# Kernel optimization log

Measured on AMD Instinct MI355X. Metric: run time of the kernel, lower is better.

The kernel has to match this reference:

```python
import jax, jax.numpy as jnp
import numpy as np

NUM_HEADS = 4
NEG_INF = -1e9  # finite large-negative to avoid inf*weight -> nan in head combiner


def setup_inputs() -> dict:
    key = jax.random.key(0)
    k1, k2, k3, k4, k5 = jax.random.split(key, 5)
    B, S, T = 16, 1024, 512
    Q, E = 256, 512
    src_encodings = jax.random.normal(k1, (B, S, E), dtype=jnp.float32)
    src_token_mask = jax.random.randint(k2, (B, S), 0, 2).astype(jnp.bool_)
    query_vec = jax.random.normal(k3, (T, B, Q), dtype=jnp.float32)
    # Linear(src_encoding_size, query_vec_size * numheads, bias=False)
    W_src = jax.random.normal(k4, (E, Q * NUM_HEADS), dtype=jnp.float32) * (1.0 / np.sqrt(E))
    # Linear(numheads, 1, bias=False) -> combiner vector of shape (numheads,)
    w_comb = jax.random.normal(k5, (NUM_HEADS,), dtype=jnp.float32) * 0.5
    return {"src_encodings": src_encodings, "src_token_mask": src_token_mask,
            "query_vec": query_vec, "W_src": W_src, "w_comb": w_comb}


def reference(src_encodings, src_token_mask, query_vec, W_src, w_comb):
    # project + leaky_relu: (B,S,E) @ (E,H*Q) -> (B,S,H*Q)
    proj = jax.nn.leaky_relu(src_encodings @ W_src)
    B, S, _ = proj.shape
    Q = query_vec.shape[-1]
    proj = proj.reshape(B, S, NUM_HEADS, Q)                 # (B,S,H,Q)
    # per-head attention scores against each query step: (T,B,S,H)
    scores = jnp.einsum('bshq,tbq->tbsh', proj, query_vec)
    # mask invalid source tokens along S (broadcast over T and heads)
    scores = jnp.where(src_token_mask[None, :, :, None], NEG_INF, scores)
    # multihead combiner Linear(H,1,bias=False): (T,B,S)
    weights = jnp.einsum('tbsh,h->tbs', scores, w_comb)
    return jax.nn.softmax(weights, axis=-1)
```

## Files before the change

kernel.cpp:

```cpp
#include <hip/hip_runtime.h>
#include <hip/hip_bf16.h>
#include <cstdint>

constexpr int Bn = 16;
constexpr int Sn = 1024;
constexpr int Tn = 512;
constexpr int QD = 256;
constexpr int En = 512;
constexpr int Hn = 4;
constexpr float SLOPE = 0.01f;
constexpr float NEG_INF = -1e9f;
constexpr int Mn = Bn * Sn;

typedef _Float16 f16;
typedef f16 f16x4 __attribute__((ext_vector_type(4)));
typedef f16 f16x8 __attribute__((ext_vector_type(8)));
typedef float f32x4 __attribute__((ext_vector_type(4)));

#define G2L(g, l) __builtin_amdgcn_global_load_lds(                      \
    (const __attribute__((address_space(1))) void*)(g),                  \
    (__attribute__((address_space(3))) void*)(l), 16, 0, 0)

#define VM6 asm volatile("s_waitcnt vmcnt(6)" ::: "memory")
#define VM4 asm volatile("s_waitcnt vmcnt(4)" ::: "memory")
#define VM0 asm volatile("s_waitcnt vmcnt(0)" ::: "memory")
#define LG0 asm volatile("s_waitcnt lgkmcnt(0)" ::: "memory")

__device__ __forceinline__ void do_conv_a(const float* __restrict__ src,
                                          f16* __restrict__ Ah, f16* __restrict__ Al,
                                          int bid, int tid) {
    const size_t i4 = (size_t)bid * 256 + tid;
    const size_t base = i4 * 4;
    const float4 v = *(const float4*)(src + base);
    f16x4 hi, lo;
    const float xs[4] = {v.x, v.y, v.z, v.w};
    #pragma unroll
    for (int j = 0; j < 4; ++j) {
        f16 h = (f16)xs[j];
        hi[j] = h;
        lo[j] = (f16)(xs[j] - (float)h);
    }
    *(f16x4*)(Ah + base) = hi;
    *(f16x4*)(Al + base) = lo;
}

__device__ __forceinline__ void do_conv_b(const float* __restrict__ W,
                                          f16* __restrict__ Bht, f16* __restrict__ Blt,
                                          float (*T)[65], int nb, int tid) {
    const int n0 = (nb & 15) * 64;
    const int k0 = (nb >> 4) * 64;
    #pragma unroll
    for (int p = 0; p < 4; ++p) {
        const int e = p * 256 + tid;
        const int r = e >> 4;
        const int c4 = e & 15;
        const float4 v = *(const float4*)(W + (size_t)(k0 + r) * (Hn * QD) + n0 + c4 * 4);
        T[r][c4 * 4 + 0] = v.x; T[r][c4 * 4 + 1] = v.y;
        T[r][c4 * 4 + 2] = v.z; T[r][c4 * 4 + 3] = v.w;
    }
    __syncthreads();
    #pragma unroll
    for (int p = 0; p < 4; ++p) {
        const int e = p * 256 + tid;
        const int r = e >> 4;
        const int c4 = e & 15;
        f16x4 hi, lo;
        #pragma unroll
        for (int j = 0; j < 4; ++j) {
            const float x = T[c4 * 4 + j][r];
            f16 h = (f16)x;
            hi[j] = h;
            lo[j] = (f16)(x - (float)h);
        }
        const size_t off = (size_t)(n0 + r) * En + k0 + c4 * 4;
        *(f16x4*)(Bht + off) = hi;
        *(f16x4*)(Blt + off) = lo;
    }
}

__device__ __forceinline__ void do_conv_q(const float* __restrict__ query,
                                          f16* __restrict__ Qh, f16* __restrict__ Ql,
                                          int qb, int tid) {
    const int rloc = tid >> 6;
    const int lane = tid & 63;
    const int row = qb * 4 + rloc;
    const int t = row >> 4, b = row & 15;
    const float4 v = *(const float4*)(query + (size_t)row * QD + lane * 4);
    f16x4 hi, lo;
    const float xs[4] = {v.x, v.y, v.z, v.w};
    #pragma unroll
    for (int j = 0; j < 4; ++j) {
        f16 h = (f16)xs[j];
        hi[j] = h;
        lo[j] = (f16)(xs[j] - (float)h);
    }
    const size_t off = ((size_t)(b * Tn + t)) * QD + lane * 4;
    *(f16x4*)(Qh + off) = hi;
    *(f16x4*)(Ql + off) = lo;
}

__device__ __forceinline__ void do_detect(const unsigned char* __restrict__ mask_bytes,
                                          int* __restrict__ flag,
                                          int* cnt, int tid) {
    if (tid == 0) *cnt = 0;
    __syncthreads();
    int local = 0;
    for (int p = tid; p < 4096; p += 256) {
        if ((p & 3) != 0 && mask_bytes[p] != 0) local++;
    }
    atomicAdd(cnt, local);
    __syncthreads();
    if (tid == 0) flag[0] = (*cnt == 0) ? 1 : 0;
}

__global__ __launch_bounds__(256) void prep_all_kernel(
    const float* __restrict__ src, const float* __restrict__ W,
    const float* __restrict__ query,
    const unsigned char* __restrict__ mask_bytes,
    f16* __restrict__ Ah, f16* __restrict__ Al,
    f16* __restrict__ Bht, f16* __restrict__ Blt,
    f16* __restrict__ Qh, f16* __restrict__ Ql,
    int* __restrict__ flag)
{
    __shared__ float T[64][65];
    __shared__ int cnt;
    const int bid = blockIdx.x;
    const int tid = threadIdx.x;
    if (bid < 8192)       do_conv_a(src, Ah, Al, bid, tid);
    else if (bid < 8320)  do_conv_b(W, Bht, Blt, T, bid - 8192, tid);
    else if (bid < 10368) do_conv_q(query, Qh, Ql, bid - 8320, tid);
    else                  do_detect(mask_bytes, flag, &cnt, tid);
}

__global__ __launch_bounds__(256) void prep_kernel(
    const float* __restrict__ src, const float* __restrict__ W,
    const unsigned char* __restrict__ mask_bytes,
    f16* __restrict__ Ah, f16* __restrict__ Al,
    f16* __restrict__ Bht, f16* __restrict__ Blt,
    int* __restrict__ flag)
{
    __shared__ float T[64][65];
    __shared__ int cnt;
    const int bid = blockIdx.x;
    const int tid = threadIdx.x;
    if (bid < 8192)      do_conv_a(src, Ah, Al, bid, tid);
    else if (bid < 8320) do_conv_b(W, Bht, Blt, T, bid - 8192, tid);
    else                 do_detect(mask_bytes, flag, &cnt, tid);
}

__global__ __launch_bounds__(256) void conv_q_kernel(
    const float* __restrict__ query, f16* __restrict__ Qh, f16* __restrict__ Ql)
{
    do_conv_q(query, Qh, Ql, blockIdx.x, threadIdx.x);
}

__global__ __launch_bounds__(256) void gemm1_kernel(
    const f16* __restrict__ Ah, const f16* __restrict__ Al,
    const f16* __restrict__ Bht, const f16* __restrict__ Blt,
    const float* __restrict__ wcomb,
    f16* __restrict__ Ch, f16* __restrict__ Cl)
{
    __shared__ f16 lds_f[36864];

    const int tid = threadIdx.x;
    const int l  = tid & 63;
    const int wv = tid >> 6;
    const int wm = wv >> 1;
    const int wn = wv & 1;

    const int bid = blockIdx.x;
    const int swz = (bid & 7) * 64 + (bid >> 3);
    const int m0 = (swz >> 2) * 128;
    const int q0 = (swz & 3) * 64;

    const int rc  = tid >> 2;
    const int xk  = ((tid & 3) ^ ((tid >> 3) & 3)) * 8;
    const int stgA = (m0 + rc) * En + xk;
    const int stgB = (q0 + rc) * En + xk;

    const int xf  = (l >> 1) & 3;
    const int kx  = ((l >> 4) ^ xf) * 8;
    const int aFrag = (wm * 64 + (l & 15)) * 32 + kx;
    const int bFrag = 4096 + (wn * 32 + (l & 15)) * 32 + kx;

    f32x4 acc[4][8];
    #pragma unroll
    for (int m = 0; m < 4; ++m)
        #pragma unroll
        for (int f = 0; f < 8; ++f) acc[m][f] = (f32x4){0.f, 0.f, 0.f, 0.f};

    auto stage1 = [&](int t) {
        const f16* As = (t < 16) ? Ah : ((t < 32) ? Al : Ah);
        const f16* Bs = (t < 32) ? Bht : Blt;
        const int kofs = (t & 15) * 32;
        f16* dst = lds_f + (t % 3) * 12288 + wv * 512;
        G2L(As + stgA + kofs,                dst);
        G2L(As + stgA + 64 * En + kofs,      dst + 2048);
        G2L(Bs + stgB + kofs,                dst + 4096);
        G2L(Bs + stgB + QD * En + kofs,      dst + 4096 + 2048);
        G2L(Bs + stgB + 2 * QD * En + kofs,  dst + 4096 + 4096);
        G2L(Bs + stgB + 3 * QD * En + kofs,  dst + 4096 + 6144);
    };

    stage1(0);
    stage1(1);
    VM6;
    __builtin_amdgcn_s_barrier();

    #pragma unroll
    for (int t = 0; t < 48; ++t) {
        if (t + 2 < 48) stage1(t + 2);
        const f16* Lb = lds_f + (t % 3) * 12288;
        f16x8 af[4], bfr[8];
        #pragma unroll
        for (int m = 0; m < 4; ++m) af[m] = *(const f16x8*)(Lb + aFrag + m * 512);
        #pragma unroll
        for (int f = 0; f < 8; ++f)
            bfr[f] = *(const f16x8*)(Lb + bFrag + (f >> 1) * 2048 + (f & 1) * 512);
        __builtin_amdgcn_s_setprio(1);
        #pragma unroll
        for (int m = 0; m < 4; ++m) {
            #pragma unroll
            for (int f = 0; f < 8; ++f)
                acc[m][f] = __builtin_amdgcn_mfma_f32_16x16x32_f16(
                    af[m], bfr[f], acc[m][f], 0, 0, 0);
        }
        __builtin_amdgcn_s_setprio(0);
        if (t <= 45)      VM6;
        else if (t == 46) VM0;
        LG0;
        __builtin_amdgcn_s_barrier();
    }

    const float w0 = wcomb[0], w1 = wcomb[1], w2 = wcomb[2], w3 = wcomb[3];
    const int rbase = m0 + wm * 64 + (l >> 4) * 4;
    #pragma unroll
    for (int m = 0; m < 4; ++m) {
        #pragma unroll
        for (int qs = 0; qs < 2; ++qs) {
            const int q = q0 + wn * 32 + qs * 16 + (l & 15);
            #pragma unroll
            for (int i = 0; i < 4; ++i) {
                float x0 = acc[m][0 + qs][i]; x0 = x0 >= 0.f ? x0 : SLOPE * x0;
                float x1 = acc[m][2 + qs][i]; x1 = x1 >= 0.f ? x1 : SLOPE * x1;
                float x2 = acc[m][4 + qs][i]; x2 = x2 >= 0.f ? x2 : SLOPE * x2;
                float x3 = acc[m][6 + qs][i]; x3 = x3 >= 0.f ? x3 : SLOPE * x3;
                const float c = w0 * x0 + w1 * x1 + w2 * x2 + w3 * x3;
                const f16 ch = (f16)c;
                const f16 cl = (f16)(c - (float)ch);
                const size_t off = (size_t)(rbase + m * 16 + i) * QD + q;
                Ch[off] = ch;
                Cl[off] = cl;
            }
        }
    }
}

__global__ __launch_bounds__(256) void gemm2_kernel(
    const f16* __restrict__ Ch, const f16* __restrict__ Cl,
    const f16* __restrict__ Qh, const f16* __restrict__ Ql,
    const void* __restrict__ maskp, const float* __restrict__ wcomb,
    const int* __restrict__ flag,
    float* __restrict__ out)
{
    __shared__ f16 lds2[24576];

    const int tid = threadIdx.x;
    const int l  = tid & 63;
    const int wv = tid >> 6;
    const int wm = wv >> 1;
    const int wn = wv & 1;

    const int bid = blockIdx.x;
    const int swz = (bid & 7) * 64 + (bid >> 3);
    const int b   = swz >> 5;
    const int s0  = ((swz >> 2) & 7) * 128;
    const int t0  = (swz & 3) * 128;

    const int rowc = tid >> 2;
    const int xk   = ((tid & 3) ^ ((rowc >> 1) & 3)) * 8;
    const int stgA = (b * Sn + s0 + rowc) * QD + xk;
    const int stgB = (b * Tn + t0 + rowc) * QD + xk;

    const int xf  = ((l >> 1) & 3);
    const int aFrag = (wm * 64 + (l & 15)) * 32 + (((l >> 4) ^ xf) * 8);
    const int bFrag = 4096 + (wn * 64 + (l & 15)) * 32 + (((l >> 4) ^ xf) * 8);

    f32x4 acc[4][4];
    #pragma unroll
    for (int m = 0; m < 4; ++m)
        #pragma unroll
        for (int n = 0; n < 4; ++n) acc[m][n] = (f32x4){0.f, 0.f, 0.f, 0.f};

    auto stage1 = [&](int t) {
        const f16* As = (t < 8) ? Ch : ((t < 16) ? Cl : Ch);
        const f16* Bs = (t < 16) ? Qh : Ql;
        const int kofs = (t & 7) * 32;
        f16* dst = lds2 + (t % 3) * 8192 + wv * 512;
        G2L(As + stgA + kofs,           dst);
        G2L(As + stgA + 64 * QD + kofs, dst + 2048);
        G2L(Bs + stgB + kofs,           dst + 4096);
        G2L(Bs + stgB + 64 * QD + kofs, dst + 4096 + 2048);
    };

    stage1(0);
    stage1(1);
    VM4;
    __builtin_amdgcn_s_barrier();

    #pragma unroll
    for (int kt = 0; kt < 24; ++kt) {
        if (kt + 2 < 24) stage1(kt + 2);
        const f16* Lb = lds2 + (kt % 3) * 8192;
        f16x8 af[4], bfr[4];
        #pragma unroll
        for (int m = 0; m < 4; ++m) af[m] = *(const f16x8*)(Lb + aFrag + m * 512);
        #pragma unroll
        for (int n = 0; n < 4; ++n) bfr[n] = *(const f16x8*)(Lb + bFrag + n * 512);
        __builtin_amdgcn_s_setprio(1);
        #pragma unroll
        for (int m = 0; m < 4; ++m) {
            #pragma unroll
            for (int n = 0; n < 4; ++n)
                acc[m][n] = __builtin_amdgcn_mfma_f32_16x16x32_f16(
                    af[m], bfr[n], acc[m][n], 0, 0, 0);
        }
        __builtin_amdgcn_s_setprio(0);
        if (kt <= 21)      VM4;
        else if (kt == 22) VM0;
        LG0;
        __builtin_amdgcn_s_barrier();
    }

    const float sumw = wcomb[0] + wcomb[1] + wcomb[2] + wcomb[3];
    const float maskval = NEG_INF * sumw;
    const bool is_int = (flag[0] != 0);
    const int rbase = s0 + wm * 64 + (l >> 4) * 4;

    bool msk[4][4];
    #pragma unroll
    for (int m = 0; m < 4; ++m)
        #pragma unroll
        for (int i = 0; i < 4; ++i) {
            const int idx = b * Sn + rbase + m * 16 + i;
            int mm;
            if (is_int) mm = ((const int*)maskp)[idx];
            else        mm = (int)((const unsigned char*)maskp)[idx];
            msk[m][i] = (mm != 0);
        }

    #pragma unroll
    for (int m = 0; m < 4; ++m)
        #pragma unroll
        for (int n = 0; n < 4; ++n) {
            const int t = t0 + wn * 64 + n * 16 + (l & 15);
            float vals[4];
            #pragma unroll
            for (int i = 0; i < 4; ++i)
                vals[i] = msk[m][i] ? maskval : acc[m][n][i];
            *(float4*)(out + ((size_t)t * Bn + b) * Sn + rbase + m * 16)
                = make_float4(vals[0], vals[1], vals[2], vals[3]);
        }
}

__global__ __launch_bounds__(256) void softmax_kernel(float* __restrict__ out) {
    const int bid = blockIdx.x;
    const int k = bid & 7;
    const int r = bid >> 3;
    const int b = (k << 1) | (r & 1);
    const int t = r >> 1;
    const size_t row = (size_t)t * Bn + b;
    float* p = out + row * (size_t)Sn;
    const int tid = threadIdx.x;
    const int lane = tid & 63, wave = tid >> 6;

    float4 v = ((const float4*)p)[tid];

    float m = fmaxf(fmaxf(v.x, v.y), fmaxf(v.z, v.w));
    #pragma unroll
    for (int off = 32; off; off >>= 1) m = fmaxf(m, __shfl_down(m, off));
    __shared__ float smax[4];
    __shared__ float sm_all;
    if (lane == 0) smax[wave] = m;
    __syncthreads();
    if (tid == 0) sm_all = fmaxf(fmaxf(smax[0], smax[1]), fmaxf(smax[2], smax[3]));
    __syncthreads();
    m = sm_all;

    float e0 = __expf(v.x - m), e1 = __expf(v.y - m);
    float e2 = __expf(v.z - m), e3 = __expf(v.w - m);
    float s = e0 + e1 + e2 + e3;
    #pragma unroll
    for (int off = 32; off; off >>= 1) s += __shfl_down(s, off);
    __shared__ float ssum[4];
    __shared__ float ss_all;
    if (lane == 0) ssum[wave] = s;
    __syncthreads();
    if (tid == 0) ss_all = ssum[0] + ssum[1] + ssum[2] + ssum[3];
    __syncthreads();
    const float inv = 1.0f / ss_all;

    ((float4*)p)[tid] = make_float4(e0 * inv, e1 * inv, e2 * inv, e3 * inv);
}

extern "C" void kernel_launch(void* const* d_in, const int* in_sizes, int n_in,
                              void* d_out, int out_size, void* d_ws, size_t ws_size,
                              hipStream_t stream) {
    const float* src   = (const float*)d_in[0];
    const void*  maskp = d_in[1];
    const float* query = (const float*)d_in[2];
    const float* Wsrc  = (const float*)d_in[3];
    const float* wcomb = (const float*)d_in[4];
    float* out = (float*)d_out;

    constexpr size_t MB = 1024 * 1024;
    char* ws = (char*)d_ws;
    int* flag = (int*)ws;
    f16* Ah  = (f16*)(ws + 256);
    f16* Al  = (f16*)(ws + 256 + 16 * MB);
    f16* Bht = (f16*)(ws + 256 + 32 * MB);
    f16* Blt = (f16*)(ws + 256 + 33 * MB);
    f16* Ch  = (f16*)(ws + 256 + 34 * MB);
    f16* Cl  = (f16*)(ws + 256 + 42 * MB);

    const bool big_ws = (ws_size >= 58 * MB + 256);

    if (big_ws) {
        f16* Qh = (f16*)(ws + 256 + 50 * MB);
        f16* Ql = (f16*)(ws + 256 + 54 * MB);
        prep_all_kernel<<<10369, 256, 0, stream>>>(
            src, Wsrc, query, (const unsigned char*)maskp,
            Ah, Al, Bht, Blt, Qh, Ql, flag);
        gemm1_kernel<<<512, 256, 0, stream>>>(Ah, Al, Bht, Blt, wcomb, Ch, Cl);
        gemm2_kernel<<<512, 256, 0, stream>>>(Ch, Cl, Qh, Ql, maskp, wcomb, flag, out);
        softmax_kernel<<<Tn * Bn, 256, 0, stream>>>(out);
    } else {
        f16* Qh = (f16*)(ws + 256);
        f16* Ql = (f16*)(ws + 256 + 4 * MB);
        prep_kernel<<<8321, 256, 0, stream>>>(
            src, Wsrc, (const unsigned char*)maskp, Ah, Al, Bht, Blt, flag);
        gemm1_kernel<<<512, 256, 0, stream>>>(Ah, Al, Bht, Blt, wcomb, Ch, Cl);
        conv_q_kernel<<<(Tn * Bn) / 4, 256, 0, stream>>>(query, Qh, Ql);
        gemm2_kernel<<<512, 256, 0, stream>>>(Ch, Cl, Qh, Ql, maskp, wcomb, flag, out);
        softmax_kernel<<<Tn * Bn, 256, 0, stream>>>(out);
    }
}
```

Baseline: 108.6 us.

## Fuse prep, both GEMMs and softmax into one cooperative persistent kernel

Replaces the four-kernel sequence (prep, gemm1, gemm2, softmax) with a single cooperative kernel of 512 blocks that runs each stage in turn, separated by grid.sync barriers. The goal is to remove kernel launch gaps and tail effects between stages. In exchange, every stage is forced onto a fixed 512-block grid at 2 blocks per CU, and the grid-wide barriers add their own cost. If the cooperative launch fails, it falls back to separate kernels.

```diff
diff --git a/kernel.cpp b/kernel.cpp
--- a/kernel.cpp
+++ b/kernel.cpp
@@ -1,6 +1,9 @@
 #include <hip/hip_runtime.h>
 #include <hip/hip_bf16.h>
+#include <hip/hip_cooperative_groups.h>
 #include <cstdint>
+
+namespace cg = cooperative_groups;
 
 constexpr int Bn = 16;
 constexpr int Sn = 1024;
@@ -113,23 +116,265 @@
     if (tid == 0) flag[0] = (*cnt == 0) ? 1 : 0;
 }
 
-__global__ __launch_bounds__(256) void prep_all_kernel(
+__global__ __launch_bounds__(256, 2) void fused_kernel(
     const float* __restrict__ src, const float* __restrict__ W,
-    const float* __restrict__ query,
-    const unsigned char* __restrict__ mask_bytes,
+    const float* __restrict__ query, const void* __restrict__ maskp,
+    const float* __restrict__ wcomb,
     f16* __restrict__ Ah, f16* __restrict__ Al,
     f16* __restrict__ Bht, f16* __restrict__ Blt,
     f16* __restrict__ Qh, f16* __restrict__ Ql,
-    int* __restrict__ flag)
+    f16* __restrict__ Ch, f16* __restrict__ Cl,
+    int* __restrict__ flag, float* __restrict__ out)
 {
-    __shared__ float T[64][65];
-    __shared__ int cnt;
+    __shared__ f16 lds_f[36864];
+    __shared__ int s_cnt;
+    cg::grid_group grid = cg::this_grid();
     const int bid = blockIdx.x;
     const int tid = threadIdx.x;
-    if (bid < 8192)       do_conv_a(src, Ah, Al, bid, tid);
-    else if (bid < 8320)  do_conv_b(W, Bht, Blt, T, bid - 8192, tid);
-    else if (bid < 10368) do_conv_q(query, Qh, Ql, bid - 8320, tid);
-    else                  do_detect(mask_bytes, flag, &cnt, tid);
+
+    #pragma unroll 4
+    for (int j = 0; j < 16; ++j) do_conv_a(src, Ah, Al, bid * 16 + j, tid);
+    #pragma unroll
+    for (int j = 0; j < 4; ++j) do_conv_q(query, Qh, Ql, bid * 4 + j, tid);
+    if (bid < 128)
+        do_conv_b(W, Bht, Blt, reinterpret_cast<float(*)[65]>(lds_f), bid, tid);
+    if (bid == 511)
+        do_detect((const unsigned char*)maskp, flag, &s_cnt, tid);
+    grid.sync();
+
+    {
+        const int l  = tid & 63;
+        const int wv = tid >> 6;
+        const int wm = wv >> 1;
+        const int wn = wv & 1;
+
+        const int swz = (bid & 7) * 64 + (bid >> 3);
+        const int m0 = (swz >> 2) * 128;
+        const int q0 = (swz & 3) * 64;
+
+        const int rc  = tid >> 2;
+        const int xk  = ((tid & 3) ^ ((tid >> 3) & 3)) * 8;
+        const int stgA = (m0 + rc) * En + xk;
+        const int stgB = (q0 + rc) * En + xk;
+
+        const int xf  = (l >> 1) & 3;
+        const int kx  = ((l >> 4) ^ xf) * 8;
+        const int aFrag = (wm * 64 + (l & 15)) * 32 + kx;
+        const int bFrag = 4096 + (wn * 32 + (l & 15)) * 32 + kx;
+
+        f32x4 acc[4][8];
+        #pragma unroll
+        for (int m = 0; m < 4; ++m)
+            #pragma unroll
+            for (int f = 0; f < 8; ++f) acc[m][f] = (f32x4){0.f, 0.f, 0.f, 0.f};
+
+        auto stage1 = [&](int t) {
+            const f16* As = (t < 16) ? Ah : ((t < 32) ? Al : Ah);
+            const f16* Bs = (t < 32) ? Bht : Blt;
+            const int kofs = (t & 15) * 32;
+            f16* dst = lds_f + (t % 3) * 12288 + wv * 512;
+            G2L(As + stgA + kofs,                dst);
+            G2L(As + stgA + 64 * En + kofs,      dst + 2048);
+            G2L(Bs + stgB + kofs,                dst + 4096);
+            G2L(Bs + stgB + QD * En + kofs,      dst + 4096 + 2048);
+            G2L(Bs + stgB + 2 * QD * En + kofs,  dst + 4096 + 4096);
+            G2L(Bs + stgB + 3 * QD * En + kofs,  dst + 4096 + 6144);
+        };
+
+        stage1(0);
+        stage1(1);
+        VM6;
+        __builtin_amdgcn_s_barrier();
+
+        #pragma unroll
+        for (int t = 0; t < 48; ++t) {
+            if (t + 2 < 48) stage1(t + 2);
+            const f16* Lb = lds_f + (t % 3) * 12288;
+            f16x8 af[4], bfr[8];
+            #pragma unroll
+            for (int m = 0; m < 4; ++m) af[m] = *(const f16x8*)(Lb + aFrag + m * 512);
+            #pragma unroll
+            for (int f = 0; f < 8; ++f)
+                bfr[f] = *(const f16x8*)(Lb + bFrag + (f >> 1) * 2048 + (f & 1) * 512);
+            __builtin_amdgcn_s_setprio(1);
+            #pragma unroll
+            for (int m = 0; m < 4; ++m) {
+                #pragma unroll
+                for (int f = 0; f < 8; ++f)
+                    acc[m][f] = __builtin_amdgcn_mfma_f32_16x16x32_f16(
+                        af[m], bfr[f], acc[m][f], 0, 0, 0);
+            }
+            __builtin_amdgcn_s_setprio(0);
+            if (t <= 45)      VM6;
+            else if (t == 46) VM0;
+            LG0;
+            __builtin_amdgcn_s_barrier();
+        }
+
+        const float w0 = wcomb[0], w1 = wcomb[1], w2 = wcomb[2], w3 = wcomb[3];
+        const int rbase = m0 + wm * 64 + (l >> 4) * 4;
+        #pragma unroll
+        for (int m = 0; m < 4; ++m) {
+            #pragma unroll
+            for (int qs = 0; qs < 2; ++qs) {
+                const int q = q0 + wn * 32 + qs * 16 + (l & 15);
+                #pragma unroll
+                for (int i = 0; i < 4; ++i) {
+                    float x0 = acc[m][0 + qs][i]; x0 = x0 >= 0.f ? x0 : SLOPE * x0;
+                    float x1 = acc[m][2 + qs][i]; x1 = x1 >= 0.f ? x1 : SLOPE * x1;
+                    float x2 = acc[m][4 + qs][i]; x2 = x2 >= 0.f ? x2 : SLOPE * x2;
+                    float x3 = acc[m][6 + qs][i]; x3 = x3 >= 0.f ? x3 : SLOPE * x3;
+                    const float c = w0 * x0 + w1 * x1 + w2 * x2 + w3 * x3;
+                    const f16 ch = (f16)c;
+                    const f16 cl = (f16)(c - (float)ch);
+                    const size_t off = (size_t)(rbase + m * 16 + i) * QD + q;
+                    Ch[off] = ch;
+                    Cl[off] = cl;
+                }
+            }
+        }
+    }
+    grid.sync();
+
+    {
+        const int l  = tid & 63;
+        const int wv = tid >> 6;
+        const int wm = wv >> 1;
+        const int wn = wv & 1;
+
+        const int swz = (bid & 7) * 64 + (bid >> 3);
+        const int b   = swz >> 5;
+        const int s0  = ((swz >> 2) & 7) * 128;
+        const int t0  = (swz & 3) * 128;
+
+        const int rowc = tid >> 2;
+        const int xk   = ((tid & 3) ^ ((rowc >> 1) & 3)) * 8;
+        const int stgA = (b * Sn + s0 + rowc) * QD + xk;
+        const int stgB = (b * Tn + t0 + rowc) * QD + xk;
+
+        const int xf  = ((l >> 1) & 3);
+        const int aFrag = (wm * 64 + (l & 15)) * 32 + (((l >> 4) ^ xf) * 8);
+        const int bFrag = 4096 + (wn * 64 + (l & 15)) * 32 + (((l >> 4) ^ xf) * 8);
+
+        f32x4 acc[4][4];
+        #pragma unroll
+        for (int m = 0; m < 4; ++m)
+            #pragma unroll
+            for (int n = 0; n < 4; ++n) acc[m][n] = (f32x4){0.f, 0.f, 0.f, 0.f};
+
+        auto stage1 = [&](int t) {
+            const f16* As = (t < 8) ? Ch : ((t < 16) ? Cl : Ch);
+            const f16* Bs = (t < 16) ? Qh : Ql;
+            const int kofs = (t & 7) * 32;
+            f16* dst = lds_f + (t % 3) * 8192 + wv * 512;
+            G2L(As + stgA + kofs,           dst);
+            G2L(As + stgA + 64 * QD + kofs, dst + 2048);
+            G2L(Bs + stgB + kofs,           dst + 4096);
+            G2L(Bs + stgB + 64 * QD + kofs, dst + 4096 + 2048);
+        };
+
+        stage1(0);
+        stage1(1);
+        VM4;
+        __builtin_amdgcn_s_barrier();
+
+        #pragma unroll
+        for (int kt = 0; kt < 24; ++kt) {
+            if (kt + 2 < 24) stage1(kt + 2);
+            const f16* Lb = lds_f + (kt % 3) * 8192;
+            f16x8 af[4], bfr[4];
+            #pragma unroll
+            for (int m = 0; m < 4; ++m) af[m] = *(const f16x8*)(Lb + aFrag + m * 512);
+            #pragma unroll
+            for (int n = 0; n < 4; ++n) bfr[n] = *(const f16x8*)(Lb + bFrag + n * 512);
+            __builtin_amdgcn_s_setprio(1);
+            #pragma unroll
+            for (int m = 0; m < 4; ++m) {
+                #pragma unroll
+                for (int n = 0; n < 4; ++n)
+                    acc[m][n] = __builtin_amdgcn_mfma_f32_16x16x32_f16(
+                        af[m], bfr[n], acc[m][n], 0, 0, 0);
+            }
+            __builtin_amdgcn_s_setprio(0);
+            if (kt <= 21)      VM4;
+            else if (kt == 22) VM0;
+            LG0;
+            __builtin_amdgcn_s_barrier();
+        }
+
+        const float sumw = wcomb[0] + wcomb[1] + wcomb[2] + wcomb[3];
+        const float maskval = NEG_INF * sumw;
+        const bool is_int = (flag[0] != 0);
+        const int rbase = s0 + wm * 64 + (l >> 4) * 4;
+
+        bool msk[4][4];
+        #pragma unroll
+        for (int m = 0; m < 4; ++m)
+            #pragma unroll
+            for (int i = 0; i < 4; ++i) {
+                const int idx = b * Sn + rbase + m * 16 + i;
+                int mm;
+                if (is_int) mm = ((const int*)maskp)[idx];
+                else        mm = (int)((const unsigned char*)maskp)[idx];
+                msk[m][i] = (mm != 0);
+            }
+
+        #pragma unroll
+        for (int m = 0; m < 4; ++m)
+            #pragma unroll
+            for (int n = 0; n < 4; ++n) {
+                const int t = t0 + wn * 64 + n * 16 + (l & 15);
+                float vals[4];
+                #pragma unroll
+                for (int i = 0; i < 4; ++i)
+                    vals[i] = msk[m][i] ? maskval : acc[m][n][i];
+                *(float4*)(out + ((size_t)t * Bn + b) * Sn + rbase + m * 16)
+                    = make_float4(vals[0], vals[1], vals[2], vals[3]);
+            }
+    }
+    grid.sync();
+
+    {
+        const int k   = bid & 7;
+        const int idx = bid >> 3;
+        const int b   = 2 * k + (idx >> 5);
+        const int ih  = idx & 31;
+        const int lane = tid & 63, wvv = tid >> 6;
+        for (int p4 = 0; p4 < 4; ++p4) {
+            const int t = ih * 16 + p4 * 4 + wvv;
+            float* p = out + ((size_t)t * Bn + b) * Sn;
+            float4 v[4];
+            #pragma unroll
+            for (int i = 0; i < 4; ++i) v[i] = ((const float4*)p)[lane + 64 * i];
+
+            float m = v[0].x;
+            #pragma unroll
+            for (int i = 0; i < 4; ++i) {
+                m = fmaxf(m, fmaxf(fmaxf(v[i].x, v[i].y), fmaxf(v[i].z, v[i].w)));
+            }
+            #pragma unroll
+            for (int off = 32; off; off >>= 1) m = fmaxf(m, __shfl_down(m, off));
+            m = __shfl(m, 0);
+
+            float4 e[4];
+            float s = 0.f;
+            #pragma unroll
+            for (int i = 0; i < 4; ++i) {
+                e[i].x = __expf(v[i].x - m); e[i].y = __expf(v[i].y - m);
+                e[i].z = __expf(v[i].z - m); e[i].w = __expf(v[i].w - m);
+                s += e[i].x + e[i].y + e[i].z + e[i].w;
+            }
+            #pragma unroll
+            for (int off = 32; off; off >>= 1) s += __shfl_down(s, off);
+            s = __shfl(s, 0);
+            const float inv = 1.0f / s;
+
+            #pragma unroll
+            for (int i = 0; i < 4; ++i)
+                ((float4*)p)[lane + 64 * i] = make_float4(
+                    e[i].x * inv, e[i].y * inv, e[i].z * inv, e[i].w * inv);
+        }
+    }
 }
 
 __global__ __launch_bounds__(256) void prep_kernel(
@@ -428,10 +673,18 @@
     if (big_ws) {
         f16* Qh = (f16*)(ws + 256 + 50 * MB);
         f16* Ql = (f16*)(ws + 256 + 54 * MB);
-        prep_all_kernel<<<10369, 256, 0, stream>>>(
-            src, Wsrc, query, (const unsigned char*)maskp,
-            Ah, Al, Bht, Blt, Qh, Ql, flag);
+        void* args[] = {
+            (void*)&src, (void*)&Wsrc, (void*)&query, (void*)&maskp,
+            (void*)&wcomb, (void*)&Ah, (void*)&Al, (void*)&Bht, (void*)&Blt,
+            (void*)&Qh, (void*)&Ql, (void*)&Ch, (void*)&Cl,
+            (void*)&flag, (void*)&out};
+        hipError_t err = hipLaunchCooperativeKernel(
+            (const void*)fused_kernel, dim3(512), dim3(256), args, 0, stream);
+        if (err == hipSuccess) return;
+        prep_kernel<<<8321, 256, 0, stream>>>(
+            src, Wsrc, (const unsigned char*)maskp, Ah, Al, Bht, Blt, flag);
         gemm1_kernel<<<512, 256, 0, stream>>>(Ah, Al, Bht, Blt, wcomb, Ch, Cl);
+        conv_q_kernel<<<(Tn * Bn) / 4, 256, 0, stream>>>(query, Qh, Ql);
         gemm2_kernel<<<512, 256, 0, stream>>>(Ch, Cl, Qh, Ql, maskp, wcomb, flag, out);
         softmax_kernel<<<Tn * Bn, 256, 0, stream>>>(out);
     } else {
```

Result: slower. 335.4 us (+208.8%).
